# Kernel tuning notes

Measured on AMD Instinct MI355X. Metric: run time of the kernel, lower is better.

Reference implementation:

```python
import jax, jax.numpy as jnp
import numpy as np

DIM = 2048
NUM_HEADS = 16
HEAD_DIM = DIM // NUM_HEADS
BATCH, SEQ = 2, 2048


def setup_inputs() -> dict:
    key = jax.random.key(0)
    kx, kq, kk, kv, ko = jax.random.split(key, 5)
    scale = 1.0 / np.sqrt(DIM)
    return {
        "x": jax.random.normal(kx, (BATCH, SEQ, DIM), dtype=jnp.float32),
        "Wq": jax.random.normal(kq, (DIM, DIM), dtype=jnp.float32) * scale,
        "Wk": jax.random.normal(kk, (DIM, DIM), dtype=jnp.float32) * scale,
        "Wv": jax.random.normal(kv, (DIM, DIM), dtype=jnp.float32) * scale,
        "Wo": jax.random.normal(ko, (DIM, DIM), dtype=jnp.float32) * scale,
    }


def reference(x, Wq, Wk, Wv, Wo):
    b, s, _ = x.shape
    # QKV projections (flax Dense, no bias): y = x @ W
    q = (x @ Wq).reshape(b, s, NUM_HEADS, HEAD_DIM)
    k = (x @ Wk).reshape(b, s, NUM_HEADS, HEAD_DIM)
    v = (x @ Wv).reshape(b, s, NUM_HEADS, HEAD_DIM)
    # full (non-causal) softmax attention, scores are [b, h, q, k]
    scores = jnp.einsum('bqhd,bkhd->bhqk', q, k) * (HEAD_DIM ** -0.5)
    attn = jax.nn.softmax(scores, axis=-1)
    out = jnp.einsum('bhqk,bkhd->bqhd', attn, v).reshape(b, s, DIM)
    return out @ Wo
```

## Files before the change

kernel.cpp:

```cpp
#include <hip/hip_runtime.h>
#include <stdint.h>


typedef unsigned short u16;
typedef __attribute__((ext_vector_type(8))) short bf16x8;
typedef __attribute__((ext_vector_type(4))) float f32x4;
typedef __attribute__((ext_vector_type(2))) unsigned int u32x2;

__device__ __forceinline__ u16 f2bf(float f) {
  union { float f; uint32_t u; } v; v.f = f;
  return (u16)((v.u + 0x7fffu + ((v.u >> 16) & 1u)) >> 16);
}

__device__ __forceinline__ float fast_exp2(float x) {
#if __has_builtin(__builtin_amdgcn_exp2f)
  return __builtin_amdgcn_exp2f(x);
#else
  return exp2f(x);
#endif
}

__device__ __forceinline__ void gl_lds16(const void* g, void* l) {
  __builtin_amdgcn_global_load_lds(
      (const __attribute__((address_space(1))) unsigned int*)g,
      (__attribute__((address_space(3))) unsigned int*)l, 16, 0, 0);
}

__global__ __launch_bounds__(256) void sniff_k(const u16* __restrict__ x,
                                               int* __restrict__ flag) {
  __shared__ int cnt;
  const int t = threadIdx.x;
  if (t == 0) cnt = 0;
  __syncthreads();
  int sane = 0;
#pragma unroll
  for (int i = 0; i < 16; ++i) {
    u16 u = x[t * 16 + i];
    int e = (u >> 7) & 0xff;
    sane += (e >= 90 && e <= 150) ? 1 : 0;
  }
  atomicAdd(&cnt, sane);
  __syncthreads();
  if (t == 0) *flag = (cnt >= 3700) ? 0 : 1;
}

__global__ __launch_bounds__(256) void convert_x_k(const void* __restrict__ xin,
                                                   u16* __restrict__ xb,
                                                   const int* __restrict__ flag) {
  if (*flag == 0) return;
  const int i = (blockIdx.x * 256 + threadIdx.x) * 8;
  const float* xf = (const float*)xin;
  float4 a = *(const float4*)(xf + i);
  float4 b = *(const float4*)(xf + i + 4);
  bf16x8 o;
  o[0] = (short)f2bf(a.x); o[1] = (short)f2bf(a.y);
  o[2] = (short)f2bf(a.z); o[3] = (short)f2bf(a.w);
  o[4] = (short)f2bf(b.x); o[5] = (short)f2bf(b.y);
  o[6] = (short)f2bf(b.z); o[7] = (short)f2bf(b.w);
  *(bf16x8*)(xb + i) = o;
}

__global__ __launch_bounds__(256) void convert_transpose_k(const void* __restrict__ w0,
                                                           const void* __restrict__ w1,
                                                           const void* __restrict__ w2,
                                                           const void* __restrict__ w3,
                                                           u16* __restrict__ out_base,
                                                           const int* __restrict__ flag) {
  __shared__ u16 tile[64][66];
  const int z = blockIdx.z;
  const void* in = (z == 0) ? w0 : (z == 1) ? w1 : (z == 2) ? w2 : w3;
  u16* out = out_base + (size_t)z * 4194304u;
  const int tr = blockIdx.y, tc = blockIdx.x, t = threadIdx.x;
  if (*flag) {
    const float* inf32 = (const float*)in;
#pragma unroll
    for (int i = 0; i < 16; ++i) {
      int idx = t + i * 256, r = idx >> 6, c = idx & 63;
      tile[r][c] = f2bf(inf32[(size_t)(tr * 64 + r) * 2048 + tc * 64 + c]);
    }
  } else {
    const u16* inb = (const u16*)in;
#pragma unroll
    for (int i = 0; i < 16; ++i) {
      int idx = t + i * 256, r = idx >> 6, c = idx & 63;
      tile[r][c] = inb[(size_t)(tr * 64 + r) * 2048 + tc * 64 + c];
    }
  }
  __syncthreads();
#pragma unroll
  for (int i = 0; i < 16; ++i) {
    int idx = t + i * 256, r = idx >> 6, c = idx & 63;
    out[(size_t)(tc * 64 + r) * 2048 + tr * 64 + c] = tile[c][r];
  }
}

__global__ __launch_bounds__(256) void transpose_k(const u16* __restrict__ in,
                                                   u16* __restrict__ out) {
  __shared__ u16 tile[64][66];
  const size_t zoff = (size_t)blockIdx.z * 4194304u;
  in += zoff; out += zoff;
  const int tr = blockIdx.y, tc = blockIdx.x, t = threadIdx.x;
#pragma unroll
  for (int i = 0; i < 16; ++i) {
    int idx = t + i * 256, r = idx >> 6, c = idx & 63;
    tile[r][c] = in[(size_t)(tr * 64 + r) * 2048 + tc * 64 + c];
  }
  __syncthreads();
#pragma unroll
  for (int i = 0; i < 16; ++i) {
    int idx = t + i * 256, r = idx >> 6, c = idx & 63;
    out[(size_t)(tc * 64 + r) * 2048 + tr * 64 + c] = tile[c][r];
  }
}

__global__ __launch_bounds__(512, 2) void gemm256(const u16* __restrict__ A,
                                                  const void* __restrict__ Araw,
                                                  const int* __restrict__ aflag,
                                                  const u16* __restrict__ Bt,
                                                  u16* __restrict__ Cbase,
                                                  float qscale) {
  __shared__ __align__(16) u16 Ls[2][2][256 * 64];

  const int t = threadIdx.x, wave = t >> 6, lane = t & 63;
  const int g = lane >> 4, lq = lane & 15;
  const int wr = wave >> 2, wc = wave & 3;
  const int bid = blockIdx.x;
  const int swz = (bid & 7) * 48 + (bid >> 3);
  const int bm = swz / 24, bn = swz % 24;

  const u16* Ause = (*aflag == 0) ? (const u16*)Araw : A;
  const u16* Arow = Ause + (size_t)(bm * 256) * 2048;
  const u16* Brow = Bt + (size_t)(bn * 256) * 2048;
  const int lr = lane >> 3, lcs = ((lane & 7) ^ lr) * 8;

  int cofs[2];
#pragma unroll
  for (int kk = 0; kk < 2; ++kk) cofs[kk] = ((kk * 4 + g) ^ (lq & 7)) * 8;

  f32x4 acc[8][4];
#pragma unroll
  for (int i = 0; i < 8; ++i)
#pragma unroll
    for (int j = 0; j < 4; ++j) acc[i][j] = f32x4{0.f, 0.f, 0.f, 0.f};

  auto stage = [&](int tt) {
    u16* Al = &Ls[tt & 1][0][0];
    u16* Bl = &Ls[tt & 1][1][0];
    const int kb = tt * 64;
#pragma unroll
    for (int i = 0; i < 4; ++i) {
      const int s = wave * 4 + i;
      gl_lds16(Arow + (size_t)(s * 8 + lr) * 2048 + kb + lcs, Al + s * 8 * 64);
      gl_lds16(Brow + (size_t)(s * 8 + lr) * 2048 + kb + lcs, Bl + s * 8 * 64);
    }
  };

  stage(0);
  stage(1);

  for (int kt = 0; kt < 32; ++kt) {
    if (kt < 31) asm volatile("s_waitcnt vmcnt(8)" ::: "memory");
    else         asm volatile("s_waitcnt vmcnt(0)" ::: "memory");
    __builtin_amdgcn_sched_barrier(0);
    __builtin_amdgcn_s_barrier();

    const u16* Al = &Ls[kt & 1][0][0];
    const u16* Bl = &Ls[kt & 1][1][0];

    bf16x8 af[8], bf0[4], bf1[4];
#pragma unroll
    for (int m = 0; m < 4; ++m)
#pragma unroll
      for (int kk = 0; kk < 2; ++kk)
        af[m * 2 + kk] = *(const bf16x8*)(&Al[(wr * 128 + m * 16 + lq) * 64 + cofs[kk]]);
#pragma unroll
    for (int n = 0; n < 2; ++n)
#pragma unroll
      for (int kk = 0; kk < 2; ++kk)
        bf0[n * 2 + kk] = *(const bf16x8*)(&Bl[(wc * 64 + n * 16 + lq) * 64 + cofs[kk]]);
    __builtin_amdgcn_s_setprio(1);
#pragma unroll
    for (int m = 0; m < 4; ++m)
#pragma unroll
      for (int n = 0; n < 2; ++n)
#pragma unroll
        for (int kk = 0; kk < 2; ++kk)
          acc[m][n] = __builtin_amdgcn_mfma_f32_16x16x32_bf16(af[m * 2 + kk], bf0[n * 2 + kk], acc[m][n], 0, 0, 0);
    __builtin_amdgcn_s_setprio(0);
#pragma unroll
    for (int n = 0; n < 2; ++n)
#pragma unroll
      for (int kk = 0; kk < 2; ++kk)
        bf1[n * 2 + kk] = *(const bf16x8*)(&Bl[(wc * 64 + (2 + n) * 16 + lq) * 64 + cofs[kk]]);
    __builtin_amdgcn_s_setprio(1);
#pragma unroll
    for (int m = 0; m < 4; ++m)
#pragma unroll
      for (int n = 0; n < 2; ++n)
#pragma unroll
        for (int kk = 0; kk < 2; ++kk)
          acc[m][2 + n] = __builtin_amdgcn_mfma_f32_16x16x32_bf16(af[m * 2 + kk], bf1[n * 2 + kk], acc[m][2 + n], 0, 0, 0);
    __builtin_amdgcn_s_setprio(0);
#pragma unroll
    for (int m = 0; m < 4; ++m)
#pragma unroll
      for (int kk = 0; kk < 2; ++kk)
        af[m * 2 + kk] = *(const bf16x8*)(&Al[(wr * 128 + (4 + m) * 16 + lq) * 64 + cofs[kk]]);
    __builtin_amdgcn_s_setprio(1);
#pragma unroll
    for (int m = 0; m < 4; ++m)
#pragma unroll
      for (int n = 0; n < 2; ++n)
#pragma unroll
        for (int kk = 0; kk < 2; ++kk)
          acc[4 + m][2 + n] = __builtin_amdgcn_mfma_f32_16x16x32_bf16(af[m * 2 + kk], bf1[n * 2 + kk], acc[4 + m][2 + n], 0, 0, 0);
    __builtin_amdgcn_s_setprio(0);
    __builtin_amdgcn_s_setprio(1);
#pragma unroll
    for (int m = 0; m < 4; ++m)
#pragma unroll
      for (int n = 0; n < 2; ++n)
#pragma unroll
        for (int kk = 0; kk < 2; ++kk)
          acc[4 + m][n] = __builtin_amdgcn_mfma_f32_16x16x32_bf16(af[m * 2 + kk], bf0[n * 2 + kk], acc[4 + m][n], 0, 0, 0);
    __builtin_amdgcn_s_setprio(0);

    asm volatile("s_waitcnt lgkmcnt(0)" ::: "memory");
    __builtin_amdgcn_sched_barrier(0);
    __builtin_amdgcn_s_barrier();
    if (kt < 30) stage(kt + 2);
  }

  const int which = bn >> 3;
  u16* C = Cbase + (size_t)which * 2u * 4194304u;
  const float scale = (which == 0) ? qscale : 1.0f;
  const int colbase = (bn & 7) * 256 + wc * 64;
#pragma unroll
  for (int m = 0; m < 8; ++m)
#pragma unroll
    for (int n = 0; n < 4; ++n)
#pragma unroll
      for (int j = 0; j < 4; ++j) {
        size_t row = (size_t)(bm * 256 + wr * 128 + m * 16 + g * 4 + j);
        size_t col = (size_t)(colbase + n * 16 + lq);
        C[row * 2048 + col] = f2bf(acc[m][n][j] * scale);
      }
}

__global__ __launch_bounds__(256) void gemm_bt(const u16* __restrict__ A,
                                               const void* __restrict__ Araw,
                                               const int* __restrict__ aflag,
                                               const u16* __restrict__ Bt,
                                               u16* __restrict__ C0,
                                               u16* __restrict__ C1,
                                               u16* __restrict__ C2,
                                               float qscale,
                                               const int* __restrict__ outflag) {
  __shared__ u16 As[128 * 64];
  __shared__ u16 Bs[128 * 64];
  const int bx = blockIdx.x, by = blockIdx.y, t = threadIdx.x;
  const int wave = t >> 6, lane = t & 63;
  const int g = lane >> 4, lq = lane & 15;
  const int wr = wave >> 1, wc = wave & 1;
  const int which = bx >> 4, nb = bx & 15;
  u16* C = (which == 0) ? C0 : ((which == 1) ? C1 : C2);
  const float scale = (which == 0) ? qscale : 1.0f;
  const u16* Ause = (aflag && *aflag == 0) ? (const u16*)Araw : A;
  const int lr = lane >> 3, lcs = ((lane & 7) ^ lr) * 8;

  const u16* Arow = Ause + (size_t)(by * 128) * 2048;
  const u16* Brow = Bt + (size_t)(bx * 128) * 2048;

  int cofs[2];
#pragma unroll
  for (int ks = 0; ks < 2; ++ks) cofs[ks] = ((ks * 4 + g) ^ (lq & 7)) * 8;

  f32x4 acc[4][4];
#pragma unroll
  for (int i = 0; i < 4; ++i)
#pragma unroll
    for (int j = 0; j < 4; ++j) acc[i][j] = f32x4{0.f, 0.f, 0.f, 0.f};

  for (int kb = 0; kb < 2048; kb += 64) {
    __syncthreads();
#pragma unroll
    for (int i = 0; i < 4; ++i) {
      const int r = wave * 32 + i * 8;
      gl_lds16(Arow + (size_t)(r + lr) * 2048 + kb + lcs, &As[r * 64]);
      gl_lds16(Brow + (size_t)(r + lr) * 2048 + kb + lcs, &Bs[r * 64]);
    }
    __syncthreads();
#pragma unroll
    for (int ks = 0; ks < 2; ++ks) {
      bf16x8 af[4], bfr[4];
#pragma unroll
      for (int mt = 0; mt < 4; ++mt)
        af[mt] = *(const bf16x8*)(&As[(wr * 64 + mt * 16 + lq) * 64 + cofs[ks]]);
#pragma unroll
      for (int nt = 0; nt < 4; ++nt)
        bfr[nt] = *(const bf16x8*)(&Bs[(wc * 64 + nt * 16 + lq) * 64 + cofs[ks]]);
#pragma unroll
      for (int mt = 0; mt < 4; ++mt)
#pragma unroll
        for (int nt = 0; nt < 4; ++nt)
          acc[mt][nt] = __builtin_amdgcn_mfma_f32_16x16x32_bf16(af[mt], bfr[nt], acc[mt][nt], 0, 0, 0);
    }
  }
  const int outF32 = outflag ? *outflag : 0;
#pragma unroll
  for (int mt = 0; mt < 4; ++mt)
#pragma unroll
    for (int nt = 0; nt < 4; ++nt)
#pragma unroll
      for (int j = 0; j < 4; ++j) {
        size_t row = (size_t)(by * 128 + wr * 64 + mt * 16 + g * 4 + j);
        size_t col = (size_t)(nb * 128 + wc * 64 + nt * 16 + lq);
        float v = acc[mt][nt][j] * scale;
        if (outF32) ((float*)C)[row * 2048 + col] = v;
        else C[row * 2048 + col] = f2bf(v);
      }
}

__global__ __launch_bounds__(256, 4) void attn_kernel(const u16* __restrict__ Q,
                                                      const u16* __restrict__ K,
                                                      const u16* __restrict__ Vt,
                                                      u16* __restrict__ O) {
  __shared__ u16 Ks[64 * 128];
  __shared__ u16 Vs[128 * 64];

  const int qb = blockIdx.x, h = blockIdx.y, b = blockIdx.z;
  const int t = threadIdx.x, wave = t >> 6, lane = t & 63;
  const int g = lane >> 4, lq = lane & 15;

  const size_t qk_base = ((size_t)b * 2048) * 2048 + (size_t)h * 128;
  const size_t vt_base = ((size_t)b * 2048 + (size_t)h * 128) * 2048;

  bf16x8 qf[4];
  {
    const u16* qp = Q + qk_base + (size_t)(qb * 64 + wave * 16 + lq) * 2048 + g * 8;
#pragma unroll
    for (int kk = 0; kk < 4; ++kk) qf[kk] = *(const bf16x8*)(qp + kk * 32);
  }

  f32x4 acc_o[8];
#pragma unroll
  for (int i = 0; i < 8; ++i) acc_o[i] = f32x4{0.f, 0.f, 0.f, 0.f};
  float l_run = 0.f;

  const int vlr = lane >> 3, vlcs = ((lane & 7) ^ vlr) * 8;

  int kofs[4];
#pragma unroll
  for (int kk = 0; kk < 4; ++kk) kofs[kk] = ((kk * 4 + g) ^ (lq & 7)) * 8;

  for (int kb = 0; kb < 2048; kb += 64) {
    __syncthreads();
#pragma unroll
    for (int i = 0; i < 4; ++i) {
      const int win = wave * 2 + (i >> 1), half = i & 1;
      const int kr = half * 4 + (lane >> 4);
      const int kc = (lane & 15) ^ kr;
      gl_lds16(K + qk_base + (size_t)(kb + win * 8 + kr) * 2048 + kc * 8,
               &Ks[win * 1024 + half * 512]);
      const int vr = wave * 32 + i * 8;
      gl_lds16(Vt + vt_base + (size_t)(vr + vlr) * 2048 + kb + vlcs,
               &Vs[vr * 64]);
    }
    __syncthreads();

    f32x4 st[4];
#pragma unroll
    for (int mt = 0; mt < 4; ++mt) st[mt] = f32x4{0.f, 0.f, 0.f, 0.f};
#pragma unroll
    for (int kk = 0; kk < 4; ++kk)
#pragma unroll
      for (int mt = 0; mt < 4; ++mt) {
        bf16x8 af = *(const bf16x8*)(&Ks[(mt * 16 + lq) * 128 + kofs[kk]]);
        st[mt] = __builtin_amdgcn_mfma_f32_16x16x32_bf16(af, qf[kk], st[mt], 0, 0, 0);
      }

    uint32_t c[4][2];
#pragma unroll
    for (int mt = 0; mt < 4; ++mt) {
      float p0 = fast_exp2(st[mt][0]);
      float p1 = fast_exp2(st[mt][1]);
      float p2 = fast_exp2(st[mt][2]);
      float p3 = fast_exp2(st[mt][3]);
      l_run += (p0 + p1) + (p2 + p3);
      asm("v_cvt_pk_bf16_f32 %0, %1, %2" : "=v"(c[mt][0]) : "v"(p0), "v"(p1));
      asm("v_cvt_pk_bf16_f32 %0, %1, %2" : "=v"(c[mt][1]) : "v"(p2), "v"(p3));
    }

#pragma unroll
    for (int kk = 0; kk < 2; ++kk) {
      u32x2 s0 = __builtin_amdgcn_permlane32_swap(c[2 * kk][0], c[2 * kk + 1][0], false, false);
      u32x2 r0 = __builtin_amdgcn_permlane16_swap(s0[0], s0[1], false, false);
      u32x2 s1 = __builtin_amdgcn_permlane32_swap(c[2 * kk][1], c[2 * kk + 1][1], false, false);
      u32x2 r1 = __builtin_amdgcn_permlane16_swap(s1[0], s1[1], false, false);
      union { uint32_t d[4]; bf16x8 v; } af;
      af.d[0] = r0[0];
      af.d[1] = r1[0];
      af.d[2] = r0[1];
      af.d[3] = r1[1];
#pragma unroll
      for (int nt = 0; nt < 8; ++nt) {
        bf16x8 bfr = *(const bf16x8*)(&Vs[(nt * 16 + lq) * 64 + ((kk * 4 + g) ^ (lq & 7)) * 8]);
        acc_o[nt] = __builtin_amdgcn_mfma_f32_16x16x32_bf16(af.v, bfr, acc_o[nt], 0, 0, 0);
      }
    }
  }

  l_run += __shfl_xor(l_run, 16);
  l_run += __shfl_xor(l_run, 32);
  const float i0 = 1.f / __shfl(l_run, g * 4 + 0);
  const float i1 = 1.f / __shfl(l_run, g * 4 + 1);
  const float i2 = 1.f / __shfl(l_run, g * 4 + 2);
  const float i3 = 1.f / __shfl(l_run, g * 4 + 3);
  u16* op = O + ((size_t)b * 2048 + qb * 64 + wave * 16) * 2048 + h * 128;
#pragma unroll
  for (int nt = 0; nt < 8; ++nt) {
    op[(size_t)(g * 4 + 0) * 2048 + nt * 16 + lq] = f2bf(acc_o[nt][0] * i0);
    op[(size_t)(g * 4 + 1) * 2048 + nt * 16 + lq] = f2bf(acc_o[nt][1] * i1);
    op[(size_t)(g * 4 + 2) * 2048 + nt * 16 + lq] = f2bf(acc_o[nt][2] * i2);
    op[(size_t)(g * 4 + 3) * 2048 + nt * 16 + lq] = f2bf(acc_o[nt][3] * i3);
  }
}

extern "C" void kernel_launch(void* const* d_in, const int* in_sizes, int n_in,
                              void* d_out, int out_size, void* d_ws, size_t ws_size,
                              hipStream_t stream) {
  const void* x  = d_in[0];
  const void* Wq = d_in[1];
  const void* Wk = d_in[2];
  const void* Wv = d_in[3];
  const void* Wo = d_in[4];
  u16* ws = (u16*)d_ws;

  const size_t SLOT = 4194304u;
  u16* xb  = ws + 0 * SLOT;
  u16* WqT = ws + 2 * SLOT;
  u16* WoT = ws + 5 * SLOT;
  u16* Qb  = ws + 6 * SLOT;
  u16* Kb  = ws + 8 * SLOT;
  u16* Vb  = ws + 10 * SLOT;
  int* flag = (int*)(ws + 12 * SLOT);
  u16* VTd = (u16*)d_out;
  u16* Ab  = Qb;

  sniff_k<<<1, 256, 0, stream>>>((const u16*)x, flag);

  convert_x_k<<<4096, 256, 0, stream>>>(x, xb, flag);
  convert_transpose_k<<<dim3(32, 32, 4), 256, 0, stream>>>(Wq, Wk, Wv, Wo, WqT, flag);

  const float QSCALE = 0.12751745f;
  gemm256<<<384, 512, 0, stream>>>(xb, x, flag, WqT, Qb, QSCALE);

  transpose_k<<<dim3(32, 32, 2), 256, 0, stream>>>(Vb, VTd);

  attn_kernel<<<dim3(32, 16, 2), dim3(256), 0, stream>>>(Qb, Kb, VTd, Ab);

  gemm_bt<<<dim3(16, 32), 256, 0, stream>>>(Ab, Ab, nullptr, WoT,
                                            (u16*)d_out, (u16*)d_out, (u16*)d_out,
                                            1.0f, flag);
}
```

Before: 416.7 us.

## Split GEMM LDS tiles into halves and interleave staged loads with MFMA quadrants

```diff
diff --git a/kernel.cpp b/kernel.cpp
--- a/kernel.cpp
+++ b/kernel.cpp
@@ -119,7 +119,7 @@
                                                   const u16* __restrict__ Bt,
                                                   u16* __restrict__ Cbase,
                                                   float qscale) {
-  __shared__ __align__(16) u16 Ls[2][2][256 * 64];
+  __shared__ __align__(16) u16 Ls[2][2][2][128 * 64];
 
   const int t = threadIdx.x, wave = t >> 6, lane = t & 63;
   const int g = lane >> 4, lq = lane & 15;
@@ -143,108 +143,109 @@
 #pragma unroll
     for (int j = 0; j < 4; ++j) acc[i][j] = f32x4{0.f, 0.f, 0.f, 0.f};
 
-  auto stage = [&](int tt) {
-    u16* Al = &Ls[tt & 1][0][0];
-    u16* Bl = &Ls[tt & 1][1][0];
+  auto stageH = [&](int tt, int mat, int h) {
+    const u16* src = mat ? Brow : Arow;
+    u16* dst = &Ls[tt & 1][mat][h][0];
     const int kb = tt * 64;
 #pragma unroll
-    for (int i = 0; i < 4; ++i) {
-      const int s = wave * 4 + i;
-      gl_lds16(Arow + (size_t)(s * 8 + lr) * 2048 + kb + lcs, Al + s * 8 * 64);
-      gl_lds16(Brow + (size_t)(s * 8 + lr) * 2048 + kb + lcs, Bl + s * 8 * 64);
+    for (int i = 0; i < 2; ++i) {
+      const int s = wave * 2 + i;
+      gl_lds16(src + (size_t)(h * 128 + s * 8 + lr) * 2048 + kb + lcs,
+               dst + s * 8 * 64);
     }
   };
 
-  stage(0);
-  stage(1);
-
-  for (int kt = 0; kt < 32; ++kt) {
-    if (kt < 31) asm volatile("s_waitcnt vmcnt(8)" ::: "memory");
+  bf16x8 af[8], bfr[4];
+  auto ldA = [&](const u16* base) {
+#pragma unroll
+    for (int m = 0; m < 4; ++m)
+#pragma unroll
+      for (int kk = 0; kk < 2; ++kk)
+        af[m * 2 + kk] = *(const bf16x8*)(&base[(wr * 64 + m * 16 + lq) * 64 + cofs[kk]]);
+  };
+  auto ldB = [&](const u16* base) {
+#pragma unroll
+    for (int n = 0; n < 2; ++n)
+#pragma unroll
+      for (int kk = 0; kk < 2; ++kk)
+        bfr[n * 2 + kk] = *(const bf16x8*)(&base[(wc * 32 + n * 16 + lq) * 64 + cofs[kk]]);
+  };
+  auto mmac = [&](int mh, int nh) {
+    __builtin_amdgcn_s_barrier();
+    asm volatile("s_waitcnt lgkmcnt(0)" ::: "memory");
+    __builtin_amdgcn_sched_barrier(0);
+    __builtin_amdgcn_s_setprio(1);
+#pragma unroll
+    for (int m = 0; m < 4; ++m)
+#pragma unroll
+      for (int n = 0; n < 2; ++n)
+#pragma unroll
+        for (int kk = 0; kk < 2; ++kk)
+          acc[mh * 4 + m][nh * 2 + n] = __builtin_amdgcn_mfma_f32_16x16x32_bf16(
+              af[m * 2 + kk], bfr[n * 2 + kk], acc[mh * 4 + m][nh * 2 + n], 0, 0, 0);
+    __builtin_amdgcn_s_setprio(0);
+    __builtin_amdgcn_s_barrier();
+  };
+
+  stageH(0, 0, 0); stageH(0, 1, 0); stageH(0, 0, 1); stageH(0, 1, 1);
+  stageH(1, 0, 0); stageH(1, 1, 0);
+  asm volatile("s_waitcnt vmcnt(4)" ::: "memory");
+  __builtin_amdgcn_sched_barrier(0);
+  __builtin_amdgcn_s_barrier();
+
+  for (int it = 0; it < 16; ++it) {
+    const int u1 = 2 * it + 1, u2 = 2 * it + 2, u3 = 2 * it + 3;
+    ldA(&Ls[0][0][0][0]);
+    ldB(&Ls[0][1][0][0]);
+    stageH(u1, 0, 1); stageH(u1, 1, 1);
+    mmac(0, 0);
+    ldB(&Ls[0][1][1][0]);
+    mmac(0, 1);
+    ldA(&Ls[0][0][1][0]);
+    ldB(&Ls[0][1][0][0]);
+    if (u2 < 32) stageH(u2, 0, 0);
+    mmac(1, 0);
+    ldB(&Ls[0][1][1][0]);
+    if (u2 < 32) stageH(u2, 1, 0);
+    if (it < 15) asm volatile("s_waitcnt vmcnt(4)" ::: "memory");
     else         asm volatile("s_waitcnt vmcnt(0)" ::: "memory");
     __builtin_amdgcn_sched_barrier(0);
-    __builtin_amdgcn_s_barrier();
-
-    const u16* Al = &Ls[kt & 1][0][0];
-    const u16* Bl = &Ls[kt & 1][1][0];
-
-    bf16x8 af[8], bf0[4], bf1[4];
-#pragma unroll
-    for (int m = 0; m < 4; ++m)
-#pragma unroll
-      for (int kk = 0; kk < 2; ++kk)
-        af[m * 2 + kk] = *(const bf16x8*)(&Al[(wr * 128 + m * 16 + lq) * 64 + cofs[kk]]);
-#pragma unroll
-    for (int n = 0; n < 2; ++n)
-#pragma unroll
-      for (int kk = 0; kk < 2; ++kk)
-        bf0[n * 2 + kk] = *(const bf16x8*)(&Bl[(wc * 64 + n * 16 + lq) * 64 + cofs[kk]]);
-    __builtin_amdgcn_s_setprio(1);
-#pragma unroll
-    for (int m = 0; m < 4; ++m)
-#pragma unroll
-      for (int n = 0; n < 2; ++n)
-#pragma unroll
-        for (int kk = 0; kk < 2; ++kk)
-          acc[m][n] = __builtin_amdgcn_mfma_f32_16x16x32_bf16(af[m * 2 + kk], bf0[n * 2 + kk], acc[m][n], 0, 0, 0);
-    __builtin_amdgcn_s_setprio(0);
-#pragma unroll
-    for (int n = 0; n < 2; ++n)
-#pragma unroll
-      for (int kk = 0; kk < 2; ++kk)
-        bf1[n * 2 + kk] = *(const bf16x8*)(&Bl[(wc * 64 + (2 + n) * 16 + lq) * 64 + cofs[kk]]);
-    __builtin_amdgcn_s_setprio(1);
-#pragma unroll
-    for (int m = 0; m < 4; ++m)
-#pragma unroll
-      for (int n = 0; n < 2; ++n)
-#pragma unroll
-        for (int kk = 0; kk < 2; ++kk)
-          acc[m][2 + n] = __builtin_amdgcn_mfma_f32_16x16x32_bf16(af[m * 2 + kk], bf1[n * 2 + kk], acc[m][2 + n], 0, 0, 0);
-    __builtin_amdgcn_s_setprio(0);
-#pragma unroll
-    for (int m = 0; m < 4; ++m)
-#pragma unroll
-      for (int kk = 0; kk < 2; ++kk)
-        af[m * 2 + kk] = *(const bf16x8*)(&Al[(wr * 128 + (4 + m) * 16 + lq) * 64 + cofs[kk]]);
-    __builtin_amdgcn_s_setprio(1);
-#pragma unroll
-    for (int m = 0; m < 4; ++m)
-#pragma unroll
-      for (int n = 0; n < 2; ++n)
-#pragma unroll
-        for (int kk = 0; kk < 2; ++kk)
-          acc[4 + m][2 + n] = __builtin_amdgcn_mfma_f32_16x16x32_bf16(af[m * 2 + kk], bf1[n * 2 + kk], acc[4 + m][2 + n], 0, 0, 0);
-    __builtin_amdgcn_s_setprio(0);
-    __builtin_amdgcn_s_setprio(1);
-#pragma unroll
-    for (int m = 0; m < 4; ++m)
-#pragma unroll
-      for (int n = 0; n < 2; ++n)
-#pragma unroll
-        for (int kk = 0; kk < 2; ++kk)
-          acc[4 + m][n] = __builtin_amdgcn_mfma_f32_16x16x32_bf16(af[m * 2 + kk], bf0[n * 2 + kk], acc[4 + m][n], 0, 0, 0);
-    __builtin_amdgcn_s_setprio(0);
-
-    asm volatile("s_waitcnt lgkmcnt(0)" ::: "memory");
+    mmac(1, 1);
+    ldA(&Ls[1][0][0][0]);
+    ldB(&Ls[1][1][0][0]);
+    if (u2 < 32) { stageH(u2, 0, 1); stageH(u2, 1, 1); }
+    mmac(0, 0);
+    ldB(&Ls[1][1][1][0]);
+    mmac(0, 1);
+    ldA(&Ls[1][0][1][0]);
+    ldB(&Ls[1][1][0][0]);
+    if (u3 < 32) stageH(u3, 0, 0);
+    mmac(1, 0);
+    ldB(&Ls[1][1][1][0]);
+    if (u3 < 32) stageH(u3, 1, 0);
+    asm volatile("s_waitcnt vmcnt(4)" ::: "memory");
     __builtin_amdgcn_sched_barrier(0);
-    __builtin_amdgcn_s_barrier();
-    if (kt < 30) stage(kt + 2);
+    mmac(1, 1);
   }
 
   const int which = bn >> 3;
   u16* C = Cbase + (size_t)which * 2u * 4194304u;
   const float scale = (which == 0) ? qscale : 1.0f;
-  const int colbase = (bn & 7) * 256 + wc * 64;
-#pragma unroll
-  for (int m = 0; m < 8; ++m)
-#pragma unroll
-    for (int n = 0; n < 4; ++n)
-#pragma unroll
-      for (int j = 0; j < 4; ++j) {
-        size_t row = (size_t)(bm * 256 + wr * 128 + m * 16 + g * 4 + j);
-        size_t col = (size_t)(colbase + n * 16 + lq);
-        C[row * 2048 + col] = f2bf(acc[m][n][j] * scale);
-      }
+  const int colbase = (bn & 7) * 256;
+#pragma unroll
+  for (int mh = 0; mh < 2; ++mh)
+#pragma unroll
+    for (int m = 0; m < 4; ++m)
+#pragma unroll
+      for (int nh = 0; nh < 2; ++nh)
+#pragma unroll
+        for (int n = 0; n < 2; ++n)
+#pragma unroll
+          for (int j = 0; j < 4; ++j) {
+            size_t row = (size_t)(bm * 256 + mh * 128 + wr * 64 + m * 16 + g * 4 + j);
+            size_t col = (size_t)(colbase + nh * 128 + wc * 32 + n * 16 + lq);
+            C[row * 2048 + col] = f2bf(acc[mh * 4 + m][nh * 2 + n][j] * scale);
+          }
 }
 
 __global__ __launch_bounds__(256) void gemm_bt(const u16* __restrict__ A,
```

Result: faster. 402.3 us (-3.5%).
